# Performance work log

Hardware: AMD Instinct MI355X
Metric: run time of the kernel (lower is better)

Reference implementation:

```python
import jax, jax.numpy as jnp
import numpy as np

N = 50000   # nodes
D = 256     # embed_dim
H = 256     # hidden_dim
E = 250000  # edges per relation type
T = 3       # edge types
NEG_SLOPE = 0.2  # PyG GATConv default


def setup_inputs() -> dict:
    key = jax.random.key(0)
    ks = jax.random.split(key, 12)
    s = lambda k, shape: jax.random.normal(k, shape, jnp.float32) * 0.05
    z = jax.random.normal(ks[0], (N, D), jnp.float32)
    ei = jax.random.randint(ks[1], (T, 2, E), 0, N, dtype=jnp.int32)
    W1 = s(ks[2], (T, D, H)); as1 = s(ks[3], (T, H)); ad1 = s(ks[4], (T, H))
    b1 = jnp.zeros((T, H), jnp.float32)
    W2 = s(ks[5], (T, H, H)); as2 = s(ks[6], (T, H)); ad2 = s(ks[7], (T, H))
    b2 = jnp.zeros((T, H), jnp.float32)
    Wh = s(ks[8], (H, 1)); bh = jnp.zeros((1,), jnp.float32)
    return dict(z=z, ei=ei, W1=W1, as1=as1, ad1=ad1, b1=b1,
                W2=W2, as2=as2, ad2=ad2, b2=b2, Wh=Wh, bh=bh)


def gat_conv(x, ei, W, a_s, a_d, b):
    # PyG GATConv, heads=1, no self loops: h = x W; e_ij = leaky_relu(a_s.h_j + a_d.h_i)
    # alpha = softmax over incoming edges of node i; out_i = sum_j alpha_ij h_j + bias
    src, dst = ei[0], ei[1]
    n = x.shape[0]
    h = x @ W                              # [N, H]
    a_src = h @ a_s                        # [N]
    a_dst = h @ a_d                        # [N]
    e = jax.nn.leaky_relu(a_src[src] + a_dst[dst], NEG_SLOPE)   # [E]
    m = jax.ops.segment_max(e, dst, num_segments=n)             # per-dst max
    ex = jnp.exp(e - m[dst])
    den = jax.ops.segment_sum(ex, dst, num_segments=n)
    alpha = ex / den[dst]                                       # [E]
    out = jax.ops.segment_sum(h[src] * alpha[:, None], dst, num_segments=n)
    return out + b


def layer(x, ei, W, a_s, a_d, b):
    # sum of per-type GATConv outputs, then ReLU (matches module)
    outs = jax.vmap(lambda e_, W_, s_, d_, b_: gat_conv(x, e_, W_, s_, d_, b_))(ei, W, a_s, a_d, b)
    return jax.nn.relu(outs.sum(0))


def reference(z, ei, W1, as1, ad1, b1, W2, as2, ad2, b2, Wh, bh):
    h1 = layer(z, ei, W1, as1, ad1, b1)
    h2 = layer(h1, ei, W2, as2, ad2, b2)
    return jax.nn.sigmoid(h2 @ Wh + bh).squeeze(-1)   # [N]
```

## Files before the change

### kernel.cpp

```cpp
#include <hip/hip_runtime.h>

#define GAT_N 50000
#define GAT_D 256
#define GAT_T 3
#define GAT_E 250000
#define GAT_B (GAT_T*GAT_N)
#define GAT_TOTE (GAT_T*GAT_E)
#define GAT_COLS (GAT_T*GAT_D)
#define GAT_SLOPE 0.2f

typedef unsigned short u16;
typedef unsigned int u32;
typedef __attribute__((ext_vector_type(8))) short s16x8;
typedef __attribute__((ext_vector_type(8))) __bf16 bf16x8;
typedef __attribute__((ext_vector_type(4))) float f32x4;
typedef __attribute__((ext_vector_type(4))) u32 u32x4;

__device__ __forceinline__ u16 f2bf(float f) {
    u32 x = __builtin_bit_cast(u32, f);
    u32 r = (x + 0x7fffu + ((x >> 16) & 1u)) >> 16;
    return (u16)r;
}
__device__ __forceinline__ float lo16(u32 w) {
    return __builtin_bit_cast(float, w << 16);
}
__device__ __forceinline__ float hi16(u32 w) {
    return __builtin_bit_cast(float, w & 0xffff0000u);
}

__global__ void gat_zero(u32* __restrict__ cnt, u32* __restrict__ total) {
    int idx = blockIdx.x * 256 + threadIdx.x;
    if (idx == 0) *total = 0u;
    if (idx < GAT_B) cnt[idx] = 0u;
}

__global__ void gat_prep(const float* __restrict__ W1, const float* __restrict__ W2,
                         const float* __restrict__ z, const float* __restrict__ b1,
                         const float* __restrict__ b2, const int* __restrict__ ei,
                         u16* __restrict__ WT1b, u16* __restrict__ WT2b,
                         u16* __restrict__ zb, u32* __restrict__ cnt,
                         float* __restrict__ bias3)
{
    int idx = blockIdx.x * 256 + threadIdx.x;
    if (idx < GAT_T * GAT_D * GAT_D) {
        int t = idx >> 16, r = idx & 65535;
        int d = r >> 8, h = r & 255;
        WT1b[t * 65536 + h * 256 + d] = f2bf(W1[idx]);
        WT2b[t * 65536 + h * 256 + d] = f2bf(W2[idx]);
    }
    if (idx < 2 * GAT_D) {
        const float* bb = (idx < GAT_D) ? b1 : b2;
        int c = idx & 255;
        bias3[idx] = bb[c] + bb[GAT_D + c] + bb[2 * GAT_D + c];
    }
    if (idx < GAT_TOTE) {
        int t = idx / GAT_E;
        int e = idx - t * GAT_E;
        int dst = ei[t * 2 * GAT_E + GAT_E + e];
        atomicAdd(&cnt[dst * GAT_T + t], 1u);
    }
    if (idx < GAT_N * GAT_D / 4) {
        f32x4 v = ((const f32x4*)z)[idx];
        ushort4 pk;
        pk.x = f2bf(v.x); pk.y = f2bf(v.y); pk.z = f2bf(v.z); pk.w = f2bf(v.w);
        ((ushort4*)zb)[idx] = pk;
    }
}

__global__ void gat_alloc(const u32* __restrict__ cnt, u32* __restrict__ pos2,
                          u32* __restrict__ degp, u32* __restrict__ cur,
                          u32* __restrict__ total)
{
    int n = blockIdx.x * 256 + threadIdx.x;
    if (n >= GAT_N) return;
    u32 c0 = cnt[3 * n], c1 = cnt[3 * n + 1], c2 = cnt[3 * n + 2];
    u32 p = atomicAdd(total, c0 + c1 + c2);
    pos2[n] = p;
    degp[n] = c0 | (c1 << 8) | (c2 << 16);
    cur[3 * n]     = p;
    cur[3 * n + 1] = p + c0;
    cur[3 * n + 2] = p + c0 + c1;
}

__global__ void gat_scatter(const int* __restrict__ ei, u32* __restrict__ cur,
                            int* __restrict__ psrc)
{
    int idx = blockIdx.x * 256 + threadIdx.x;
    if (idx >= GAT_TOTE) return;
    int t = idx / GAT_E;
    int e = idx - t * GAT_E;
    int src = ei[t * 2 * GAT_E + e];
    int dst = ei[t * 2 * GAT_E + GAT_E + e];
    u32 slot = atomicAdd(&cur[dst * GAT_T + t], 1u);
    psrc[slot] = t * GAT_N + src;
}

__global__ __launch_bounds__(512, 4) void gat_gemm(
    const u16* __restrict__ A, const u16* __restrict__ WTb,
    u16* __restrict__ H, const float* __restrict__ as_in,
    const float* __restrict__ ad_in, float* __restrict__ part_src,
    float* __restrict__ part_dst)
{
    int lin = blockIdx.x;
    int g   = lin / 48;
    int rem = lin - g * 48;
    int bc  = rem >> 3;
    int br  = (g << 3) + (rem & 7);
    if (br >= 391) return;

    __shared__ u16 Als[2][128 * 64];
    __shared__ u16 Bls[2][128 * 64];
    int tid  = threadIdx.x;
    int wave = tid >> 6, lane = tid & 63;
    int quad = lane >> 4, l16 = lane & 15;
    int wm = wave & 1, wn = wave >> 1;
    int lrow = lane >> 3;
    int swz  = ((lane & 7) ^ lrow) * 8;

    size_t arow0 = (size_t)br * 128;
    size_t brow0 = (size_t)bc * 128;

    auto STAGE = [&](int buf, int ks) {
        int k0 = ks * 64;
        #pragma unroll
        for (int r = 0; r < 2; ++r) {
            int srow = wave * 16 + r * 8 + lrow;
            const u16* gA = A   + (arow0 + srow) * GAT_D + k0 + swz;
            const u16* gB = WTb + (brow0 + srow) * GAT_D + k0 + swz;
            u16* lA = &Als[buf][wave * 1024 + r * 512];
            u16* lB = &Bls[buf][wave * 1024 + r * 512];
#if defined(__has_builtin) && __has_builtin(__builtin_amdgcn_global_load_lds)
            __builtin_amdgcn_global_load_lds(
                (const __attribute__((address_space(1))) void*)gA,
                (__attribute__((address_space(3))) void*)lA, 16, 0, 0);
            __builtin_amdgcn_global_load_lds(
                (const __attribute__((address_space(1))) void*)gB,
                (__attribute__((address_space(3))) void*)lB, 16, 0, 0);
#else
            *(s16x8*)(lA + lane * 8) = *(const s16x8*)gA;
            *(s16x8*)(lB + lane * 8) = *(const s16x8*)gB;
#endif
        }
    };

    f32x4 acc[4][2] = {};

    STAGE(0, 0);
    #pragma unroll
    for (int ks = 0; ks < 4; ++ks) {
        int cur = ks & 1;
        if (ks < 3) {
            STAGE(cur ^ 1, ks + 1);
            asm volatile("s_waitcnt vmcnt(4)" ::: "memory");
        } else {
            asm volatile("s_waitcnt vmcnt(0)" ::: "memory");
        }
        __builtin_amdgcn_s_barrier();

        #pragma unroll
        for (int kk = 0; kk < 2; ++kk) {
            int csw8 = ((kk * 4 + quad) ^ (l16 & 7)) * 8;
            bf16x8 af[4], bf[2];
            #pragma unroll
            for (int i = 0; i < 4; ++i)
                af[i] = __builtin_bit_cast(bf16x8,
                    *(const s16x8*)(&Als[cur][(wm * 64 + i * 16 + l16) * 64 + csw8]));
            #pragma unroll
            for (int j = 0; j < 2; ++j)
                bf[j] = __builtin_bit_cast(bf16x8,
                    *(const s16x8*)(&Bls[cur][(wn * 32 + j * 16 + l16) * 64 + csw8]));
            #pragma unroll
            for (int i = 0; i < 4; ++i)
                #pragma unroll
                for (int j = 0; j < 2; ++j)
                    acc[i][j] = __builtin_amdgcn_mfma_f32_16x16x32_bf16(
                        af[i], bf[j], acc[i][j], 0, 0, 0);
        }
        if (ks < 3)
            __builtin_amdgcn_s_barrier();
    }

    int gcol0 = bc * 128 + wn * 32;
    int t   = gcol0 >> 8;
    int ch0 = gcol0 & 255;
    int c32 = bc * 4 + wn;
    u16* Ht = H + (size_t)t * GAT_N * GAT_D;
    int rowb = br * 128 + wm * 64 + quad * 4;
    #pragma unroll
    for (int i = 0; i < 4; ++i) {
        #pragma unroll
        for (int j = 0; j < 2; ++j) {
            int ch = ch0 + j * 16 + l16;
            #pragma unroll
            for (int r = 0; r < 4; ++r) {
                int row = rowb + i * 16 + r;
                if (row < GAT_N) Ht[(size_t)row * GAT_D + ch] = f2bf(acc[i][j][r]);
            }
        }
    }

    float asv[2], adv[2];
    #pragma unroll
    for (int j = 0; j < 2; ++j) {
        int ch = ch0 + j * 16 + l16;
        asv[j] = as_in[t * GAT_D + ch];
        adv[j] = ad_in[t * GAT_D + ch];
    }
    #pragma unroll
    for (int i = 0; i < 4; ++i) {
        float ps[4] = {}, pd[4] = {};
        #pragma unroll
        for (int j = 0; j < 2; ++j) {
            f32x4 a = acc[i][j];
            #pragma unroll
            for (int r = 0; r < 4; ++r) {
                ps[r] += a[r] * asv[j];
                pd[r] += a[r] * adv[j];
            }
        }
        #pragma unroll
        for (int d = 1; d < 16; d <<= 1) {
            #pragma unroll
            for (int r = 0; r < 4; ++r) {
                ps[r] += __shfl_xor(ps[r], d);
                pd[r] += __shfl_xor(pd[r], d);
            }
        }
        if (l16 == 0) {
            int row = rowb + i * 16;
            #pragma unroll
            for (int r = 0; r < 4; ++r) {
                if (row + r < GAT_N) {
                    part_src[(size_t)c32 * GAT_N + row + r] = ps[r];
                    part_dst[(size_t)c32 * GAT_N + row + r] = pd[r];
                }
            }
        }
    }
}

__global__ void gat_sum(const float* __restrict__ part_src,
                        const float* __restrict__ part_dst,
                        float* __restrict__ a_src, float* __restrict__ a_dst)
{
    int idx = blockIdx.x * 256 + threadIdx.x;
    if (idx >= GAT_B) return;
    int t = idx / GAT_N;
    int n = idx - t * GAT_N;
    const float* ps = part_src + (size_t)8 * t * GAT_N;
    const float* pd = part_dst + (size_t)8 * t * GAT_N;
    float s = 0.f, d = 0.f;
    #pragma unroll
    for (int c = 0; c < 8; ++c) {
        s += ps[(size_t)c * GAT_N + n];
        d += pd[(size_t)c * GAT_N + n];
    }
    a_src[idx] = s;
    a_dst[idx] = d;
}

__global__ __launch_bounds__(256) void gat_gather(
    const u32* __restrict__ pos2, const u32* __restrict__ degp,
    const int* __restrict__ psrc, const float* __restrict__ a_src,
    const float* __restrict__ a_dst, const u16* __restrict__ Hfb,
    const float* __restrict__ bias3, const float* __restrict__ Wh,
    const float* __restrict__ bh, int layer, u16* __restrict__ x2b,
    float* __restrict__ out)
{
    int n = blockIdx.x * 4 + (threadIdx.x >> 6);
    if (n >= GAT_N) return;
    int lane = threadIdx.x & 63;
    int half = lane >> 5, l32 = lane & 31;

    u32 o0 = pos2[n];
    u32 dp = degp[n];
    int d0 = dp & 255, d1 = (dp >> 8) & 255;
    int dtot = d0 + d1 + ((dp >> 16) & 255);
    if (dtot > 64) dtot = 64;

    int  j     = lane;
    bool valid = j < dtot;
    int  tj    = (j >= d0) + (j >= d0 + d1);
    int  rs    = valid ? psrc[o0 + j] : 0;
    float as   = a_src[rs];
    float adn  = a_dst[tj * GAT_N + n];
    float e = as + adn;
    e = (e > 0.f) ? e : GAT_SLOPE * e;
    float ex = valid ? __expf(e) : 0.f;

    float s0 = (tj == 0) ? ex : 0.f;
    float s1 = (tj == 1) ? ex : 0.f;
    float s2 = (tj == 2) ? ex : 0.f;
    #pragma unroll
    for (int d = 1; d < 64; d <<= 1) {
        s0 += __shfl_xor(s0, d);
        s1 += __shfl_xor(s1, d);
        s2 += __shfl_xor(s2, d);
    }
    float den = (tj == 0) ? s0 : ((tj == 1) ? s1 : s2);
    float alv = valid ? ex / den : 0.f;

    float r[8] = {};
    const u16* Hb = Hfb + l32 * 8;
    for (int k0 = 0; k0 < dtot; k0 += 8) {
        float al[4]; u32x4 w[4];
        #pragma unroll
        for (int u = 0; u < 4; ++u) {
            int j2 = k0 + 2 * u + half;
            float a = __shfl(alv, j2);
            int   rv = __shfl(rs, j2);
            bool  v = j2 < dtot;
            al[u] = v ? a : 0.f;
            rv = v ? rv : 0;
            w[u] = *(const u32x4*)(Hb + (size_t)rv * GAT_D);
        }
        #pragma unroll
        for (int u = 0; u < 4; ++u) {
            r[0] += al[u] * lo16(w[u].x); r[1] += al[u] * hi16(w[u].x);
            r[2] += al[u] * lo16(w[u].y); r[3] += al[u] * hi16(w[u].y);
            r[4] += al[u] * lo16(w[u].z); r[5] += al[u] * hi16(w[u].z);
            r[6] += al[u] * lo16(w[u].w); r[7] += al[u] * hi16(w[u].w);
        }
    }
    #pragma unroll
    for (int i = 0; i < 8; ++i) r[i] += __shfl_xor(r[i], 32);

    int c0 = l32 * 8;
    const float* b3 = bias3 + layer * GAT_D;
    float v[8];
    #pragma unroll
    for (int i = 0; i < 8; ++i) v[i] = fmaxf(r[i] + b3[c0 + i], 0.f);

    if (layer == 0) {
        if (half == 0) {
            u16 pk[8];
            #pragma unroll
            for (int i = 0; i < 8; ++i) pk[i] = f2bf(v[i]);
            *(s16x8*)(x2b + (size_t)n * GAT_D + c0) = *(s16x8*)pk;
        }
    } else {
        float wsum = 0.f;
        #pragma unroll
        for (int i = 0; i < 8; ++i) wsum += v[i] * Wh[c0 + i];
        #pragma unroll
        for (int d2 = 1; d2 < 32; d2 <<= 1) wsum += __shfl_xor(wsum, d2);
        if (lane == 0) out[n] = 1.0f / (1.0f + __expf(-(wsum + bh[0])));
    }
}

__global__ void PyGTypeSpecificGAT_80075370266775_kernel() {}

extern "C" void kernel_launch(void* const* d_in, const int* in_sizes, int n_in,
                              void* d_out, int out_size, void* d_ws, size_t ws_size,
                              hipStream_t stream)
{
    (void)in_sizes; (void)n_in; (void)out_size; (void)ws_size;
    const float* z   = (const float*)d_in[0];
    const int*   ei  = (const int*)d_in[1];
    const float* W1  = (const float*)d_in[2];
    const float* as1 = (const float*)d_in[3];
    const float* ad1 = (const float*)d_in[4];
    const float* b1  = (const float*)d_in[5];
    const float* W2  = (const float*)d_in[6];
    const float* as2 = (const float*)d_in[7];
    const float* ad2 = (const float*)d_in[8];
    const float* b2  = (const float*)d_in[9];
    const float* Wh  = (const float*)d_in[10];
    const float* bh  = (const float*)d_in[11];
    float* out = (float*)d_out;

    char* p = (char*)d_ws;
    u16*  Hfb  = (u16*)p;  p += (size_t)GAT_T * GAT_N * GAT_D * 2;
    u16*  x2b  = (u16*)p;  p += (size_t)GAT_N * GAT_D * 2;
    u16*  zb   = (u16*)p;  p += (size_t)GAT_N * GAT_D * 2;
    float* part_src = (float*)p; p += (size_t)24 * GAT_N * 4;
    float* part_dst = (float*)p; p += (size_t)24 * GAT_N * 4;
    float* a_src = (float*)p; p += (size_t)GAT_B * 4;
    float* a_dst = (float*)p; p += (size_t)GAT_B * 4;
    u32*  cnt  = (u32*)p;  p += (size_t)GAT_B * 4;
    u32*  cur  = (u32*)p;  p += (size_t)GAT_B * 4;
    u32*  pos2 = (u32*)p;  p += (size_t)GAT_N * 4;
    u32*  degp = (u32*)p;  p += (size_t)GAT_N * 4;
    u32*  total = (u32*)p; p += 256;
    int*  psrc = (int*)p;  p += (size_t)GAT_TOTE * 4;
    u16*  WT1b = (u16*)p;  p += (size_t)GAT_COLS * GAT_D * 2;
    u16*  WT2b = (u16*)p;  p += (size_t)GAT_COLS * GAT_D * 2;
    float* bias3 = (float*)p; p += 2 * GAT_D * 4;

    const int NODE_BLKS = (GAT_N + 255) / 256;
    const int EDGE_BLKS = (GAT_TOTE + 255) / 256;
    const int BUCK_BLKS = (GAT_B + 255) / 256;
    const int PREP_BLKS = (GAT_N * GAT_D / 4 + 255) / 256;

    gat_zero<<<BUCK_BLKS, 256, 0, stream>>>(cnt, total);
    gat_prep<<<PREP_BLKS, 256, 0, stream>>>(W1, W2, z, b1, b2, ei,
                                            WT1b, WT2b, zb, cnt, bias3);
    gat_alloc<<<NODE_BLKS, 256, 0, stream>>>(cnt, pos2, degp, cur, total);
    gat_scatter<<<EDGE_BLKS, 256, 0, stream>>>(ei, cur, psrc);

    const int GEMM_BLKS = 49 * 48;
    const int GATH_BLKS = GAT_N / 4;

    for (int layer = 0; layer < 2; ++layer) {
        const u16*   A   = (layer == 0) ? zb   : x2b;
        const u16*   WTb = (layer == 0) ? WT1b : WT2b;
        const float* as_ = (layer == 0) ? as1  : as2;
        const float* ad_ = (layer == 0) ? ad1  : ad2;

        gat_gemm<<<GEMM_BLKS, 512, 0, stream>>>(A, WTb, Hfb, as_, ad_,
                                                part_src, part_dst);
        gat_sum<<<BUCK_BLKS, 256, 0, stream>>>(part_src, part_dst,
                                               a_src, a_dst);
        gat_gather<<<GATH_BLKS, 256, 0, stream>>>(pos2, degp, psrc,
                                                  a_src, a_dst, Hfb, bias3,
                                                  Wh, bh, layer, x2b, out);
    }
}
```

Baseline: 435.6 us.

## Use DPP reductions, deepen gather unroll, and restructure prep/histogram kernels

Cross-lane sums within 16 lanes in the GEMM epilogue and softmax denominator now use DPP row operations instead of shuffles. The gather loop handles 16 neighbours per iteration instead of 8, putting more loads in flight at some cost in registers. The zeroing kernel is folded into prep, and the edge histogram becomes its own kernel so the counters are cleared before any atomics run. This keeps the launch count the same and may fix an ordering race in the earlier version.

Result: faster. 416.8 us (-4.3%).

```diff
diff --git a/kernel.cpp b/kernel.cpp
--- a/kernel.cpp
+++ b/kernel.cpp
@@ -28,36 +28,40 @@
     return __builtin_bit_cast(float, w & 0xffff0000u);
 }
 
-__global__ void gat_zero(u32* __restrict__ cnt, u32* __restrict__ total) {
+template<int CTRL>
+__device__ __forceinline__ float dppadd(float x) {
+    int y = __builtin_amdgcn_update_dpp(0, __builtin_bit_cast(int, x),
+                                        CTRL, 0xf, 0xf, true);
+    return x + __builtin_bit_cast(float, y);
+}
+__device__ __forceinline__ float sum16(float x) {
+    x = dppadd<0xB1>(x);
+    x = dppadd<0x4E>(x);
+    x = dppadd<0x141>(x);
+    x = dppadd<0x140>(x);
+    return x;
+}
+
+__global__ void gat_prep(const float* __restrict__ W1, const float* __restrict__ W2,
+                         const float* __restrict__ z, const float* __restrict__ b1,
+                         const float* __restrict__ b2, u16* __restrict__ WT1b,
+                         u16* __restrict__ WT2b, u16* __restrict__ zb,
+                         u32* __restrict__ cnt, u32* __restrict__ total,
+                         float* __restrict__ bias3)
+{
     int idx = blockIdx.x * 256 + threadIdx.x;
     if (idx == 0) *total = 0u;
-    if (idx < GAT_B) cnt[idx] = 0u;
-}
-
-__global__ void gat_prep(const float* __restrict__ W1, const float* __restrict__ W2,
-                         const float* __restrict__ z, const float* __restrict__ b1,
-                         const float* __restrict__ b2, const int* __restrict__ ei,
-                         u16* __restrict__ WT1b, u16* __restrict__ WT2b,
-                         u16* __restrict__ zb, u32* __restrict__ cnt,
-                         float* __restrict__ bias3)
-{
-    int idx = blockIdx.x * 256 + threadIdx.x;
     if (idx < GAT_T * GAT_D * GAT_D) {
         int t = idx >> 16, r = idx & 65535;
         int d = r >> 8, h = r & 255;
         WT1b[t * 65536 + h * 256 + d] = f2bf(W1[idx]);
         WT2b[t * 65536 + h * 256 + d] = f2bf(W2[idx]);
     }
+    if (idx < GAT_B) cnt[idx] = 0u;
     if (idx < 2 * GAT_D) {
         const float* bb = (idx < GAT_D) ? b1 : b2;
         int c = idx & 255;
         bias3[idx] = bb[c] + bb[GAT_D + c] + bb[2 * GAT_D + c];
-    }
-    if (idx < GAT_TOTE) {
-        int t = idx / GAT_E;
-        int e = idx - t * GAT_E;
-        int dst = ei[t * 2 * GAT_E + GAT_E + e];
-        atomicAdd(&cnt[dst * GAT_T + t], 1u);
     }
     if (idx < GAT_N * GAT_D / 4) {
         f32x4 v = ((const f32x4*)z)[idx];
@@ -65,6 +69,15 @@
         pk.x = f2bf(v.x); pk.y = f2bf(v.y); pk.z = f2bf(v.z); pk.w = f2bf(v.w);
         ((ushort4*)zb)[idx] = pk;
     }
+}
+
+__global__ void gat_hist(const int* __restrict__ ei, u32* __restrict__ cnt) {
+    int idx = blockIdx.x * 256 + threadIdx.x;
+    if (idx >= GAT_TOTE) return;
+    int t = idx / GAT_E;
+    int e = idx - t * GAT_E;
+    int dst = ei[t * 2 * GAT_E + GAT_E + e];
+    atomicAdd(&cnt[dst * GAT_T + t], 1u);
 }
 
 __global__ void gat_alloc(const u32* __restrict__ cnt, u32* __restrict__ pos2,
@@ -219,12 +232,9 @@
             }
         }
         #pragma unroll
-        for (int d = 1; d < 16; d <<= 1) {
-            #pragma unroll
-            for (int r = 0; r < 4; ++r) {
-                ps[r] += __shfl_xor(ps[r], d);
-                pd[r] += __shfl_xor(pd[r], d);
-            }
+        for (int r = 0; r < 4; ++r) {
+            ps[r] = sum16(ps[r]);
+            pd[r] = sum16(pd[r]);
         }
         if (l16 == 0) {
             int row = rowb + i * 16;
@@ -291,8 +301,9 @@
     float s0 = (tj == 0) ? ex : 0.f;
     float s1 = (tj == 1) ? ex : 0.f;
     float s2 = (tj == 2) ? ex : 0.f;
-    #pragma unroll
-    for (int d = 1; d < 64; d <<= 1) {
+    s0 = sum16(s0); s1 = sum16(s1); s2 = sum16(s2);
+    #pragma unroll
+    for (int d = 16; d < 64; d <<= 1) {
         s0 += __shfl_xor(s0, d);
         s1 += __shfl_xor(s1, d);
         s2 += __shfl_xor(s2, d);
@@ -302,10 +313,10 @@
 
     float r[8] = {};
     const u16* Hb = Hfb + l32 * 8;
-    for (int k0 = 0; k0 < dtot; k0 += 8) {
-        float al[4]; u32x4 w[4];
-        #pragma unroll
-        for (int u = 0; u < 4; ++u) {
+    for (int k0 = 0; k0 < dtot; k0 += 16) {
+        float al[8]; u32x4 w[8];
+        #pragma unroll
+        for (int u = 0; u < 8; ++u) {
             int j2 = k0 + 2 * u + half;
             float a = __shfl(alv, j2);
             int   rv = __shfl(rs, j2);
@@ -315,7 +326,7 @@
             w[u] = *(const u32x4*)(Hb + (size_t)rv * GAT_D);
         }
         #pragma unroll
-        for (int u = 0; u < 4; ++u) {
+        for (int u = 0; u < 8; ++u) {
             r[0] += al[u] * lo16(w[u].x); r[1] += al[u] * hi16(w[u].x);
             r[2] += al[u] * lo16(w[u].y); r[3] += al[u] * hi16(w[u].y);
             r[4] += al[u] * lo16(w[u].z); r[5] += al[u] * hi16(w[u].z);
@@ -392,9 +403,9 @@
     const int BUCK_BLKS = (GAT_B + 255) / 256;
     const int PREP_BLKS = (GAT_N * GAT_D / 4 + 255) / 256;
 
-    gat_zero<<<BUCK_BLKS, 256, 0, stream>>>(cnt, total);
-    gat_prep<<<PREP_BLKS, 256, 0, stream>>>(W1, W2, z, b1, b2, ei,
-                                            WT1b, WT2b, zb, cnt, bias3);
+    gat_prep<<<PREP_BLKS, 256, 0, stream>>>(W1, W2, z, b1, b2, WT1b, WT2b,
+                                            zb, cnt, total, bias3);
+    gat_hist<<<EDGE_BLKS, 256, 0, stream>>>(ei, cnt);
     gat_alloc<<<NODE_BLKS, 256, 0, stream>>>(cnt, pos2, degp, cur, total);
     gat_scatter<<<EDGE_BLKS, 256, 0, stream>>>(ei, cur, psrc);
 
```
